# Optimization experiments

Hardware: AMD Instinct MI355X
Metric: run time of the kernel (lower is better)

The kernel has to match this reference:

```python
import jax, jax.numpy as jnp
import numpy as np

N = 500_000   # active voxels
K = 27        # 3x3x3 kernel offsets
CIN = 32
COUT = 64
EPS = 1e-5


def setup_inputs() -> dict:
    key = jax.random.key(0)
    ks = jax.random.split(key, 9)
    x_feats = jax.random.normal(ks[0], (N, CIN), jnp.float32)
    # neighbor map: for each kernel offset k and output voxel i, index of the
    # input voxel contributing through offset k (submanifold conv, stride=1)
    nbr = jax.random.randint(ks[1], (K, N), 0, N, jnp.int32)
    s1 = 1.0 / np.sqrt(K * CIN)
    s2 = 1.0 / np.sqrt(K * COUT)
    w1 = jax.random.normal(ks[2], (K, CIN, COUT), jnp.float32) * s1
    w2 = jax.random.normal(ks[3], (K, COUT, COUT), jnp.float32) * s2
    g1 = jnp.ones((COUT,), jnp.float32)
    b1 = jnp.zeros((COUT,), jnp.float32)
    g2 = jnp.ones((COUT,), jnp.float32)
    b2 = jnp.zeros((COUT,), jnp.float32)
    wid = jax.random.normal(ks[4], (CIN, COUT), jnp.float32) * (1.0 / np.sqrt(CIN))
    gid = jnp.ones((COUT,), jnp.float32)
    bid = jnp.zeros((COUT,), jnp.float32)
    return {"x_feats": x_feats, "nbr": nbr, "w1": w1, "g1": g1, "b1": b1,
            "w2": w2, "g2": g2, "b2": b2, "wid": wid, "gid": gid, "bid": bid}


def _sparse_conv(feats, nbr, W):
    # feats [N, Cin], nbr [K, N], W [K, Cin, Cout]
    # scan over the fixed 27 kernel offsets: gather -> matmul -> accumulate
    def step(acc, kw):
        idx, w = kw
        return acc + feats[idx] @ w, None
    out0 = jnp.zeros((feats.shape[0], W.shape[-1]), feats.dtype)
    out, _ = jax.lax.scan(step, out0, (nbr, W))
    return out


def _bn(x, g, b):
    # training-mode BatchNorm1d over the voxel axis (biased variance, as torch)
    m = jnp.mean(x, axis=0)
    v = jnp.var(x, axis=0)
    return (x - m) * jax.lax.rsqrt(v + EPS) * g + b


def reference(x_feats, nbr, w1, g1, b1, w2, g2, b2, wid, gid, bid):
    h = jax.nn.relu(_bn(_sparse_conv(x_feats, nbr, w1), g1, b1))
    h = _bn(_sparse_conv(h, nbr, w2), g2, b2)
    ident = _bn(x_feats @ wid, gid, bid)
    return jax.nn.relu(h + ident)
```

## Files before the change

kernel.cpp:

```cpp
#include <hip/hip_runtime.h>

#define NV 500000
#define KOFF 27
#define CIN_ 32
#define COUT_ 64
#define EPS_ 1e-5f

typedef __attribute__((ext_vector_type(8))) _Float16 half8;
typedef __attribute__((ext_vector_type(4))) float floatx4;


__global__ void zero_stats_kernel(float* __restrict__ s) {
  if (threadIdx.x < 384) s[threadIdx.x] = 0.f;
}

__global__ __launch_bounds__(256) void cast_x_kernel(
    const float* __restrict__ x, _Float16* __restrict__ xh) {
  size_t q = (size_t)blockIdx.x * 256 + threadIdx.x;
  if (q >= (size_t)NV * CIN_ / 8) return;
  const float4* xp = (const float4*)x;
  float4 a = xp[2 * q], b = xp[2 * q + 1];
  half8 h;
  h[0] = (_Float16)a.x; h[1] = (_Float16)a.y; h[2] = (_Float16)a.z; h[3] = (_Float16)a.w;
  h[4] = (_Float16)b.x; h[5] = (_Float16)b.y; h[6] = (_Float16)b.z; h[7] = (_Float16)b.w;
  ((half8*)xh)[q] = h;
}

__global__ void wtrans_kernel(const float* __restrict__ w,
                              _Float16* __restrict__ wT, int CI) {
  int t = blockIdx.x * 256 + threadIdx.x;
  int total = KOFF * CI * COUT_;
  if (t >= total) return;
  int k = t / (CI * COUT_);
  int r = t % (CI * COUT_);
  int co = r / CI;
  int ci = r % CI;
  wT[t] = (_Float16)w[(k * CI + ci) * COUT_ + co];
}


template<int CI>
__device__ __forceinline__ void stageB(const _Float16* __restrict__ wT,
                                       _Float16* __restrict__ lds,
                                       int k0, int kp, int tid) {
  __syncthreads();
  const int segs = CI / 8;
  const int chunks = kp * COUT_ * segs;
  for (int idx = tid; idx < chunks; idx += 1024) {
    int row = idx / segs;
    int s = idx - row * segs;
    half8 v = *(const half8*)(wT + ((size_t)k0 * COUT_ + row) * CI + s * 8);
    *(half8*)(lds + (size_t)row * (CI + 8) + s * 8) = v;
  }
  __syncthreads();
}

template<int CI, int KPC, int D>
__device__ __forceinline__ void run_phase(
    const half8* __restrict__ fp, const int* __restrict__ nbr,
    const _Float16* __restrict__ lds, int k0,
    int v0, int v1, int m, int quad, floatx4 acc[2][4]) {
  constexpr int SEG = CI / 32;
  constexpr int ROWH8 = CI / 8;

  int j0[KPC], j1[KPC];
#pragma unroll
  for (int k = 0; k < KPC; ++k) {
    j0[k] = nbr[(k0 + k) * NV + v0] * ROWH8;
    j1[k] = nbr[(k0 + k) * NV + v1] * ROWH8;
  }

  half8 ring[D][2][SEG];
#pragma unroll
  for (int p = 0; p < D; ++p) {
#pragma unroll
    for (int s = 0; s < SEG; ++s) {
      ring[p][0][s] = fp[(size_t)j0[p] + s * 4 + quad];
      ring[p][1][s] = fp[(size_t)j1[p] + s * 4 + quad];
    }
  }

#pragma unroll
  for (int k = 0; k < KPC; ++k) {
    const _Float16* bk = lds + (size_t)k * COUT_ * (CI + 8);
#pragma unroll
    for (int s = 0; s < SEG; ++s) {
#pragma unroll
      for (int nf = 0; nf < 4; ++nf) {
        half8 bf = *(const half8*)(bk + (nf * 16 + m) * (CI + 8) + s * 32 + quad * 8);
        acc[0][nf] = __builtin_amdgcn_mfma_f32_16x16x32_f16(ring[k % D][0][s], bf, acc[0][nf], 0, 0, 0);
        acc[1][nf] = __builtin_amdgcn_mfma_f32_16x16x32_f16(ring[k % D][1][s], bf, acc[1][nf], 0, 0, 0);
      }
    }
    if (k + D < KPC) {
#pragma unroll
      for (int s = 0; s < SEG; ++s) {
        ring[k % D][0][s] = fp[(size_t)j0[k + D] + s * 4 + quad];
        ring[k % D][1][s] = fp[(size_t)j1[k + D] + s * 4 + quad];
      }
    }
  }
}

template<int CI, bool WF16>
__global__ __launch_bounds__(1024, 4) void conv_mfma_v3(
    const _Float16* __restrict__ feats, const int* __restrict__ nbr,
    const _Float16* __restrict__ wT, float* __restrict__ outF,
    _Float16* __restrict__ outH) {
  constexpr int LDSH = (CI == 64) ? 7 * 64 * 72 : 9 * 64 * 40;
  __shared__ __align__(16) _Float16 ldsB[LDSH];

  int tid = threadIdx.x;
  int wave = tid >> 6, lane = tid & 63;
  int m = lane & 15, quad = lane >> 4;
  int vbase = (blockIdx.x * 16 + wave) * 32;
  int v0 = vbase + m;
  int v1 = vbase + 16 + m;
  v0 = v0 < NV ? v0 : NV - 1;
  v1 = v1 < NV ? v1 : NV - 1;
  const half8* fp = (const half8*)feats;

  floatx4 acc[2][4];
#pragma unroll
  for (int g = 0; g < 2; ++g)
#pragma unroll
    for (int nf = 0; nf < 4; ++nf) acc[g][nf] = (floatx4){0.f, 0.f, 0.f, 0.f};

  if constexpr (CI == 64) {
    stageB<CI>(wT, ldsB, 0, 7, tid);
    run_phase<CI, 7, 3>(fp, nbr, ldsB, 0, v0, v1, m, quad, acc);
    stageB<CI>(wT, ldsB, 7, 7, tid);
    run_phase<CI, 7, 3>(fp, nbr, ldsB, 7, v0, v1, m, quad, acc);
    stageB<CI>(wT, ldsB, 14, 7, tid);
    run_phase<CI, 7, 3>(fp, nbr, ldsB, 14, v0, v1, m, quad, acc);
    stageB<CI>(wT, ldsB, 21, 6, tid);
    run_phase<CI, 6, 3>(fp, nbr, ldsB, 21, v0, v1, m, quad, acc);
  } else {
    stageB<CI>(wT, ldsB, 0, 9, tid);
    run_phase<CI, 9, 4>(fp, nbr, ldsB, 0, v0, v1, m, quad, acc);
    stageB<CI>(wT, ldsB, 9, 9, tid);
    run_phase<CI, 9, 4>(fp, nbr, ldsB, 9, v0, v1, m, quad, acc);
    stageB<CI>(wT, ldsB, 18, 9, tid);
    run_phase<CI, 9, 4>(fp, nbr, ldsB, 18, v0, v1, m, quad, acc);
  }

#pragma unroll
  for (int g = 0; g < 2; ++g)
#pragma unroll
    for (int nf = 0; nf < 4; ++nf)
#pragma unroll
      for (int r = 0; r < 4; ++r) {
        int row = vbase + g * 16 + quad * 4 + r;
        if (row < NV) {
          size_t o = (size_t)row * COUT_ + nf * 16 + m;
          if (WF16) outH[o] = (_Float16)acc[g][nf][r];
          else outF[o] = acc[g][nf][r];
        }
      }
}


__global__ __launch_bounds__(256) void stats_f16_kernel(
    const _Float16* __restrict__ y, float* __restrict__ sums) {
  int lane = threadIdx.x & 63;
  int r0 = blockIdx.x * 4 + (threadIdx.x >> 6);
  int stride = gridDim.x * 4;
  float s = 0.f, ss = 0.f;
  for (int r = r0; r < NV; r += stride) {
    float v = (float)y[(size_t)r * COUT_ + lane];
    s += v;
    ss = fmaf(v, v, ss);
  }
  __shared__ float ls[128];
  if (threadIdx.x < 128) ls[threadIdx.x] = 0.f;
  __syncthreads();
  atomicAdd(&ls[lane], s);
  atomicAdd(&ls[64 + lane], ss);
  __syncthreads();
  if (threadIdx.x < 128) atomicAdd(&sums[threadIdx.x], ls[threadIdx.x]);
}

__global__ __launch_bounds__(256) void stats_f32_kernel(
    const float* __restrict__ y, float* __restrict__ sums) {
  int lane = threadIdx.x & 63;
  int r0 = blockIdx.x * 4 + (threadIdx.x >> 6);
  int stride = gridDim.x * 4;
  float s = 0.f, ss = 0.f;
  for (int r = r0; r < NV; r += stride) {
    float v = y[(size_t)r * COUT_ + lane];
    s += v;
    ss = fmaf(v, v, ss);
  }
  __shared__ float ls[128];
  if (threadIdx.x < 128) ls[threadIdx.x] = 0.f;
  __syncthreads();
  atomicAdd(&ls[lane], s);
  atomicAdd(&ls[64 + lane], ss);
  __syncthreads();
  if (threadIdx.x < 128) atomicAdd(&sums[threadIdx.x], ls[threadIdx.x]);
}

__global__ __launch_bounds__(256) void ident_stats_kernel(
    const float* __restrict__ x, const float* __restrict__ wid,
    float* __restrict__ sums) {
  int lane = threadIdx.x & 63;
  int wv = blockIdx.x * 4 + (threadIdx.x >> 6);
  int nw = gridDim.x * 4;
  float wcol[CIN_];
#pragma unroll
  for (int ci = 0; ci < CIN_; ++ci) wcol[ci] = wid[ci * COUT_ + lane];
  float s = 0.f, ss = 0.f;
  for (int v = wv; v < NV; v += nw) {
    const float* xr = x + (size_t)v * CIN_;
    float d = 0.f;
#pragma unroll
    for (int ci = 0; ci < CIN_; ++ci) d = fmaf(xr[ci], wcol[ci], d);
    s += d;
    ss = fmaf(d, d, ss);
  }
  __shared__ float ls[128];
  if (threadIdx.x < 128) ls[threadIdx.x] = 0.f;
  __syncthreads();
  atomicAdd(&ls[lane], s);
  atomicAdd(&ls[64 + lane], ss);
  __syncthreads();
  if (threadIdx.x < 128) atomicAdd(&sums[threadIdx.x], ls[threadIdx.x]);
}

__global__ void finalize_kernel(const float* __restrict__ sums,
                                const float* __restrict__ g,
                                const float* __restrict__ b,
                                float* __restrict__ out) {
  int c = threadIdx.x;
  float m = sums[c] * (1.0f / NV);
  float var = sums[64 + c] * (1.0f / NV) - m * m;
  float sc = g[c] / sqrtf(var + EPS_);
  out[c] = sc;
  out[64 + c] = b[c] - m * sc;
}

__global__ __launch_bounds__(256) void bnrelu_f16_kernel(
    _Float16* __restrict__ y, const float* __restrict__ scsh) {
  size_t q = (size_t)blockIdx.x * 256 + threadIdx.x;
  if (q >= (size_t)NV * COUT_ / 8) return;
  int c0 = (int)(q & 7) * 8;
  half8 v = ((const half8*)y)[q];
#pragma unroll
  for (int jj = 0; jj < 8; ++jj) {
    float f = fmaxf(fmaf((float)v[jj], scsh[c0 + jj], scsh[64 + c0 + jj]), 0.f);
    v[jj] = (_Float16)f;
  }
  ((half8*)y)[q] = v;
}

__global__ __launch_bounds__(256) void final_kernel(
    const float* __restrict__ x, const float* __restrict__ wid,
    float* __restrict__ y2out, const float* __restrict__ ss2,
    const float* __restrict__ ssid) {
  int lane = threadIdx.x & 63;
  int wv = blockIdx.x * 4 + (threadIdx.x >> 6);
  int nw = gridDim.x * 4;
  float wcol[CIN_];
#pragma unroll
  for (int ci = 0; ci < CIN_; ++ci) wcol[ci] = wid[ci * COUT_ + lane];
  float sc2 = ss2[lane], sh2 = ss2[64 + lane];
  float sci = ssid[lane], shi = ssid[64 + lane];
  for (int v = wv; v < NV; v += nw) {
    const float* xr = x + (size_t)v * CIN_;
    float d = 0.f;
#pragma unroll
    for (int ci = 0; ci < CIN_; ++ci) d = fmaf(xr[ci], wcol[ci], d);
    size_t o = (size_t)v * COUT_ + lane;
    float r = fmaf(y2out[o], sc2, sh2) + fmaf(d, sci, shi);
    y2out[o] = fmaxf(r, 0.f);
  }
}

extern "C" void kernel_launch(void* const* d_in, const int* in_sizes, int n_in,
                              void* d_out, int out_size, void* d_ws, size_t ws_size,
                              hipStream_t stream) {
  const float* x   = (const float*)d_in[0];
  const int*   nbr = (const int*)d_in[1];
  const float* w1  = (const float*)d_in[2];
  const float* g1  = (const float*)d_in[3];
  const float* b1  = (const float*)d_in[4];
  const float* w2  = (const float*)d_in[5];
  const float* g2  = (const float*)d_in[6];
  const float* b2  = (const float*)d_in[7];
  const float* wid = (const float*)d_in[8];
  const float* gid = (const float*)d_in[9];
  const float* bid = (const float*)d_in[10];
  float* out = (float*)d_out;

  _Float16* y1h = (_Float16*)d_ws;
  _Float16* xh  = y1h + (size_t)NV * COUT_;
  _Float16* wT1 = xh + (size_t)NV * CIN_;
  _Float16* wT2 = wT1 + KOFF * COUT_ * CIN_;
  float*    st  = (float*)(wT2 + KOFF * COUT_ * COUT_);

  const int NWG = (NV + 511) / 512;

  zero_stats_kernel<<<1, 384, 0, stream>>>(st);
  cast_x_kernel<<<(NV * CIN_ / 8 + 255) / 256, 256, 0, stream>>>(x, xh);
  wtrans_kernel<<<(KOFF * CIN_ * COUT_ + 255) / 256, 256, 0, stream>>>(w1, wT1, CIN_);
  wtrans_kernel<<<(KOFF * COUT_ * COUT_ + 255) / 256, 256, 0, stream>>>(w2, wT2, COUT_);

  conv_mfma_v3<CIN_, true><<<NWG, 1024, 0, stream>>>(xh, nbr, wT1, nullptr, y1h);
  stats_f16_kernel<<<2048, 256, 0, stream>>>(y1h, st + 0);
  ident_stats_kernel<<<2048, 256, 0, stream>>>(x, wid, st + 256);
  finalize_kernel<<<1, 64, 0, stream>>>(st + 0, g1, b1, st + 384);
  finalize_kernel<<<1, 64, 0, stream>>>(st + 256, gid, bid, st + 640);
  bnrelu_f16_kernel<<<(NV * COUT_ / 8 + 255) / 256, 256, 0, stream>>>(y1h, st + 384);

  conv_mfma_v3<COUT_, false><<<NWG, 1024, 0, stream>>>(y1h, nbr, wT2, out, nullptr);
  stats_f32_kernel<<<2048, 256, 0, stream>>>(out, st + 128);
  finalize_kernel<<<1, 64, 0, stream>>>(st + 128, g2, b2, st + 512);
  final_kernel<<<4096, 256, 0, stream>>>(x, wid, out, st + 512, st + 640);
}
```

Before: 1.182 ms.

## Fuse BN statistics into conv epilogues and pre-swizzle weights into MFMA fragment order

The BatchNorm sum and sum-of-squares reductions now happen in the conv kernel epilogues, using wave shuffles and LDS atomics, so the separate passes that re-read y1 and the output are gone. The x cast to fp16 is merged into the identity-branch stats kernel, and weight transposition plus stats zeroing go into a single prep kernel. That prep kernel writes weights in per-lane MFMA fragment order, so LDS staging becomes a plain contiguous copy and B-fragment reads are conflict-free. This removes several full-tensor memory passes and kernel launches, at the cost of extra epilogue work and atomics inside the conv kernels.

```diff
diff --git a/kernel.cpp b/kernel.cpp
--- a/kernel.cpp
+++ b/kernel.cpp
@@ -10,58 +10,94 @@
 typedef __attribute__((ext_vector_type(4))) float floatx4;
 
 
-__global__ void zero_stats_kernel(float* __restrict__ s) {
-  if (threadIdx.x < 384) s[threadIdx.x] = 0.f;
-}
-
-__global__ __launch_bounds__(256) void cast_x_kernel(
-    const float* __restrict__ x, _Float16* __restrict__ xh) {
-  size_t q = (size_t)blockIdx.x * 256 + threadIdx.x;
-  if (q >= (size_t)NV * CIN_ / 8) return;
-  const float4* xp = (const float4*)x;
-  float4 a = xp[2 * q], b = xp[2 * q + 1];
+template<int CI>
+__device__ __forceinline__ void fill_chunk(const float* __restrict__ w,
+                                           half8* __restrict__ wS, int t) {
+  constexpr int SEG = CI / 32;
+  int k = t / (SEG * 256);
+  int r = t - k * SEG * 256;
+  int s = r >> 8;
+  int nf = (r >> 6) & 3;
+  int lane = r & 63;
+  int m = lane & 15, quad = lane >> 4;
+  int co = nf * 16 + m;
+  int ci0 = s * 32 + quad * 8;
   half8 h;
-  h[0] = (_Float16)a.x; h[1] = (_Float16)a.y; h[2] = (_Float16)a.z; h[3] = (_Float16)a.w;
-  h[4] = (_Float16)b.x; h[5] = (_Float16)b.y; h[6] = (_Float16)b.z; h[7] = (_Float16)b.w;
-  ((half8*)xh)[q] = h;
-}
-
-__global__ void wtrans_kernel(const float* __restrict__ w,
-                              _Float16* __restrict__ wT, int CI) {
+#pragma unroll
+  for (int j = 0; j < 8; ++j)
+    h[j] = (_Float16)w[(size_t)(k * CI + ci0 + j) * COUT_ + co];
+  wS[t] = h;
+}
+
+__global__ __launch_bounds__(256) void prep_weights(
+    const float* __restrict__ w1, const float* __restrict__ w2,
+    _Float16* __restrict__ wS1, _Float16* __restrict__ wS2,
+    float* __restrict__ st) {
   int t = blockIdx.x * 256 + threadIdx.x;
-  int total = KOFF * CI * COUT_;
-  if (t >= total) return;
-  int k = t / (CI * COUT_);
-  int r = t % (CI * COUT_);
-  int co = r / CI;
-  int ci = r % CI;
-  wT[t] = (_Float16)w[(k * CI + ci) * COUT_ + co];
-}
-
-
-template<int CI>
-__device__ __forceinline__ void stageB(const _Float16* __restrict__ wT,
-                                       _Float16* __restrict__ lds,
+  if (t < 768) st[t] = 0.f;
+  const int T1 = KOFF * 256;
+  const int T2 = KOFF * 2 * 256;
+  if (t < T1) fill_chunk<32>(w1, (half8*)wS1, t);
+  else if (t < T1 + T2) fill_chunk<64>(w2, (half8*)wS2, t - T1);
+}
+
+__global__ __launch_bounds__(256) void prep_x(
+    const float* __restrict__ x, _Float16* __restrict__ xh,
+    const float* __restrict__ wid, float* __restrict__ st) {
+  int tid = threadIdx.x, lane = tid & 63;
+  int wv = blockIdx.x * 4 + (tid >> 6);
+  int nw = gridDim.x * 4;
+  float wcol[CIN_];
+#pragma unroll
+  for (int ci = 0; ci < CIN_; ++ci) wcol[ci] = wid[ci * COUT_ + lane];
+  half8* xh8 = (half8*)xh;
+  float s = 0.f, ss = 0.f;
+  for (int v = wv; v < NV; v += nw) {
+    const float* xr = x + (size_t)v * CIN_;
+    float xv[CIN_];
+#pragma unroll
+    for (int ci = 0; ci < CIN_; ++ci) xv[ci] = xr[ci];
+    float d = 0.f;
+#pragma unroll
+    for (int ci = 0; ci < CIN_; ++ci) d = fmaf(xv[ci], wcol[ci], d);
+    if (lane < 4) {
+      half8 h;
+#pragma unroll
+      for (int j = 0; j < 8; ++j) h[j] = (_Float16)xv[lane * 8 + j];
+      xh8[(size_t)v * 4 + lane] = h;
+    }
+    s += d;
+    ss = fmaf(d, d, ss);
+  }
+  __shared__ float ls[128];
+  if (tid < 128) ls[tid] = 0.f;
+  __syncthreads();
+  atomicAdd(&ls[lane], s);
+  atomicAdd(&ls[64 + lane], ss);
+  __syncthreads();
+  if (tid < 128) atomicAdd(&st[256 + tid], ls[tid]);
+}
+
+
+template<int SEG>
+__device__ __forceinline__ void stageW(const half8* __restrict__ wS,
+                                       half8* __restrict__ lds,
                                        int k0, int kp, int tid) {
   __syncthreads();
-  const int segs = CI / 8;
-  const int chunks = kp * COUT_ * segs;
-  for (int idx = tid; idx < chunks; idx += 1024) {
-    int row = idx / segs;
-    int s = idx - row * segs;
-    half8 v = *(const half8*)(wT + ((size_t)k0 * COUT_ + row) * CI + s * 8);
-    *(half8*)(lds + (size_t)row * (CI + 8) + s * 8) = v;
-  }
+  int chunks = kp * SEG * 256;
+  const half8* src = wS + k0 * SEG * 256;
+  for (int i = tid; i < chunks; i += 1024) lds[i] = src[i];
   __syncthreads();
 }
 
 template<int CI, int KPC, int D>
 __device__ __forceinline__ void run_phase(
     const half8* __restrict__ fp, const int* __restrict__ nbr,
-    const _Float16* __restrict__ lds, int k0,
-    int v0, int v1, int m, int quad, floatx4 acc[2][4]) {
+    const half8* __restrict__ lds, int k0,
+    int v0, int v1, int lane, floatx4 acc[2][4]) {
   constexpr int SEG = CI / 32;
   constexpr int ROWH8 = CI / 8;
+  int quad = lane >> 4;
 
   int j0[KPC], j1[KPC];
 #pragma unroll
@@ -72,22 +108,20 @@
 
   half8 ring[D][2][SEG];
 #pragma unroll
-  for (int p = 0; p < D; ++p) {
+  for (int p = 0; p < D; ++p)
 #pragma unroll
     for (int s = 0; s < SEG; ++s) {
       ring[p][0][s] = fp[(size_t)j0[p] + s * 4 + quad];
       ring[p][1][s] = fp[(size_t)j1[p] + s * 4 + quad];
     }
-  }
 
 #pragma unroll
   for (int k = 0; k < KPC; ++k) {
-    const _Float16* bk = lds + (size_t)k * COUT_ * (CI + 8);
 #pragma unroll
     for (int s = 0; s < SEG; ++s) {
 #pragma unroll
       for (int nf = 0; nf < 4; ++nf) {
-        half8 bf = *(const half8*)(bk + (nf * 16 + m) * (CI + 8) + s * 32 + quad * 8);
+        half8 bf = lds[((k * SEG + s) * 4 + nf) * 64 + lane];
         acc[0][nf] = __builtin_amdgcn_mfma_f32_16x16x32_f16(ring[k % D][0][s], bf, acc[0][nf], 0, 0, 0);
         acc[1][nf] = __builtin_amdgcn_mfma_f32_16x16x32_f16(ring[k % D][1][s], bf, acc[1][nf], 0, 0, 0);
       }
@@ -103,12 +137,13 @@
 }
 
 template<int CI, bool WF16>
-__global__ __launch_bounds__(1024, 4) void conv_mfma_v3(
+__global__ __launch_bounds__(1024, 4) void conv_mfma_v4(
     const _Float16* __restrict__ feats, const int* __restrict__ nbr,
-    const _Float16* __restrict__ wT, float* __restrict__ outF,
-    _Float16* __restrict__ outH) {
-  constexpr int LDSH = (CI == 64) ? 7 * 64 * 72 : 9 * 64 * 40;
-  __shared__ __align__(16) _Float16 ldsB[LDSH];
+    const _Float16* __restrict__ wS, float* __restrict__ outF,
+    _Float16* __restrict__ outH, float* __restrict__ stats) {
+  constexpr int SEG = CI / 32;
+  constexpr int LDSH8 = (CI == 64) ? 7 * 2 * 256 : 9 * 256;
+  __shared__ half8 ldsB[LDSH8];
 
   int tid = threadIdx.x;
   int wave = tid >> 6, lane = tid & 63;
@@ -119,6 +154,7 @@
   v0 = v0 < NV ? v0 : NV - 1;
   v1 = v1 < NV ? v1 : NV - 1;
   const half8* fp = (const half8*)feats;
+  const half8* wp = (const half8*)wS;
 
   floatx4 acc[2][4];
 #pragma unroll
@@ -127,104 +163,71 @@
     for (int nf = 0; nf < 4; ++nf) acc[g][nf] = (floatx4){0.f, 0.f, 0.f, 0.f};
 
   if constexpr (CI == 64) {
-    stageB<CI>(wT, ldsB, 0, 7, tid);
-    run_phase<CI, 7, 3>(fp, nbr, ldsB, 0, v0, v1, m, quad, acc);
-    stageB<CI>(wT, ldsB, 7, 7, tid);
-    run_phase<CI, 7, 3>(fp, nbr, ldsB, 7, v0, v1, m, quad, acc);
-    stageB<CI>(wT, ldsB, 14, 7, tid);
-    run_phase<CI, 7, 3>(fp, nbr, ldsB, 14, v0, v1, m, quad, acc);
-    stageB<CI>(wT, ldsB, 21, 6, tid);
-    run_phase<CI, 6, 3>(fp, nbr, ldsB, 21, v0, v1, m, quad, acc);
+    stageW<SEG>(wp, ldsB, 0, 7, tid);
+    run_phase<CI, 7, 3>(fp, nbr, ldsB, 0, v0, v1, lane, acc);
+    stageW<SEG>(wp, ldsB, 7, 7, tid);
+    run_phase<CI, 7, 3>(fp, nbr, ldsB, 7, v0, v1, lane, acc);
+    stageW<SEG>(wp, ldsB, 14, 7, tid);
+    run_phase<CI, 7, 3>(fp, nbr, ldsB, 14, v0, v1, lane, acc);
+    stageW<SEG>(wp, ldsB, 21, 6, tid);
+    run_phase<CI, 6, 3>(fp, nbr, ldsB, 21, v0, v1, lane, acc);
   } else {
-    stageB<CI>(wT, ldsB, 0, 9, tid);
-    run_phase<CI, 9, 4>(fp, nbr, ldsB, 0, v0, v1, m, quad, acc);
-    stageB<CI>(wT, ldsB, 9, 9, tid);
-    run_phase<CI, 9, 4>(fp, nbr, ldsB, 9, v0, v1, m, quad, acc);
-    stageB<CI>(wT, ldsB, 18, 9, tid);
-    run_phase<CI, 9, 4>(fp, nbr, ldsB, 18, v0, v1, m, quad, acc);
-  }
-
-#pragma unroll
-  for (int g = 0; g < 2; ++g)
-#pragma unroll
-    for (int nf = 0; nf < 4; ++nf)
+    stageW<SEG>(wp, ldsB, 0, 9, tid);
+    run_phase<CI, 9, 4>(fp, nbr, ldsB, 0, v0, v1, lane, acc);
+    stageW<SEG>(wp, ldsB, 9, 9, tid);
+    run_phase<CI, 9, 4>(fp, nbr, ldsB, 9, v0, v1, lane, acc);
+    stageW<SEG>(wp, ldsB, 18, 9, tid);
+    run_phase<CI, 9, 4>(fp, nbr, ldsB, 18, v0, v1, lane, acc);
+  }
+
+  __syncthreads();
+  float* ls = (float*)ldsB;
+  if (tid < 128) ls[tid] = 0.f;
+  __syncthreads();
+#pragma unroll
+  for (int nf = 0; nf < 4; ++nf) {
+    float s = 0.f, ss = 0.f;
+#pragma unroll
+    for (int g = 0; g < 2; ++g)
 #pragma unroll
       for (int r = 0; r < 4; ++r) {
         int row = vbase + g * 16 + quad * 4 + r;
         if (row < NV) {
+          float v = acc[g][nf][r];
           size_t o = (size_t)row * COUT_ + nf * 16 + m;
-          if (WF16) outH[o] = (_Float16)acc[g][nf][r];
-          else outF[o] = acc[g][nf][r];
+          if (WF16) outH[o] = (_Float16)v;
+          else outF[o] = v;
+          s += v;
+          ss = fmaf(v, v, ss);
         }
       }
-}
-
-
-__global__ __launch_bounds__(256) void stats_f16_kernel(
-    const _Float16* __restrict__ y, float* __restrict__ sums) {
-  int lane = threadIdx.x & 63;
-  int r0 = blockIdx.x * 4 + (threadIdx.x >> 6);
-  int stride = gridDim.x * 4;
-  float s = 0.f, ss = 0.f;
-  for (int r = r0; r < NV; r += stride) {
-    float v = (float)y[(size_t)r * COUT_ + lane];
-    s += v;
-    ss = fmaf(v, v, ss);
-  }
-  __shared__ float ls[128];
-  if (threadIdx.x < 128) ls[threadIdx.x] = 0.f;
-  __syncthreads();
-  atomicAdd(&ls[lane], s);
-  atomicAdd(&ls[64 + lane], ss);
-  __syncthreads();
-  if (threadIdx.x < 128) atomicAdd(&sums[threadIdx.x], ls[threadIdx.x]);
-}
-
-__global__ __launch_bounds__(256) void stats_f32_kernel(
-    const float* __restrict__ y, float* __restrict__ sums) {
-  int lane = threadIdx.x & 63;
-  int r0 = blockIdx.x * 4 + (threadIdx.x >> 6);
-  int stride = gridDim.x * 4;
-  float s = 0.f, ss = 0.f;
-  for (int r = r0; r < NV; r += stride) {
-    float v = y[(size_t)r * COUT_ + lane];
-    s += v;
-    ss = fmaf(v, v, ss);
-  }
-  __shared__ float ls[128];
-  if (threadIdx.x < 128) ls[threadIdx.x] = 0.f;
-  __syncthreads();
-  atomicAdd(&ls[lane], s);
-  atomicAdd(&ls[64 + lane], ss);
-  __syncthreads();
-  if (threadIdx.x < 128) atomicAdd(&sums[threadIdx.x], ls[threadIdx.x]);
-}
-
-__global__ __launch_bounds__(256) void ident_stats_kernel(
-    const float* __restrict__ x, const float* __restrict__ wid,
-    float* __restrict__ sums) {
-  int lane = threadIdx.x & 63;
-  int wv = blockIdx.x * 4 + (threadIdx.x >> 6);
-  int nw = gridDim.x * 4;
-  float wcol[CIN_];
-#pragma unroll
-  for (int ci = 0; ci < CIN_; ++ci) wcol[ci] = wid[ci * COUT_ + lane];
-  float s = 0.f, ss = 0.f;
-  for (int v = wv; v < NV; v += nw) {
-    const float* xr = x + (size_t)v * CIN_;
-    float d = 0.f;
-#pragma unroll
-    for (int ci = 0; ci < CIN_; ++ci) d = fmaf(xr[ci], wcol[ci], d);
-    s += d;
-    ss = fmaf(d, d, ss);
-  }
-  __shared__ float ls[128];
-  if (threadIdx.x < 128) ls[threadIdx.x] = 0.f;
-  __syncthreads();
-  atomicAdd(&ls[lane], s);
-  atomicAdd(&ls[64 + lane], ss);
-  __syncthreads();
-  if (threadIdx.x < 128) atomicAdd(&sums[threadIdx.x], ls[threadIdx.x]);
+    s += __shfl_xor(s, 16, 64);
+    s += __shfl_xor(s, 32, 64);
+    ss += __shfl_xor(ss, 16, 64);
+    ss += __shfl_xor(ss, 32, 64);
+    if (quad == 0) {
+      atomicAdd(&ls[nf * 16 + m], s);
+      atomicAdd(&ls[64 + nf * 16 + m], ss);
+    }
+  }
+  __syncthreads();
+  if (tid < 128) atomicAdd(&stats[tid], ls[tid]);
+}
+
+__global__ void finalize12(float* __restrict__ st,
+                           const float* __restrict__ g1, const float* __restrict__ b1,
+                           const float* __restrict__ gid, const float* __restrict__ bid) {
+  int t = threadIdx.x;
+  int c = t & 63;
+  const float* sums = (t < 64) ? st : st + 256;
+  const float* g = (t < 64) ? g1 : gid;
+  const float* b = (t < 64) ? b1 : bid;
+  float* o = (t < 64) ? st + 384 : st + 640;
+  float m = sums[c] * (1.0f / NV);
+  float var = sums[64 + c] * (1.0f / NV) - m * m;
+  float sc = g[c] / sqrtf(var + EPS_);
+  o[c] = sc;
+  o[64 + c] = b[c] - m * sc;
 }
 
 __global__ void finalize_kernel(const float* __restrict__ sums,
@@ -294,26 +297,18 @@
 
   _Float16* y1h = (_Float16*)d_ws;
   _Float16* xh  = y1h + (size_t)NV * COUT_;
-  _Float16* wT1 = xh + (size_t)NV * CIN_;
-  _Float16* wT2 = wT1 + KOFF * COUT_ * CIN_;
-  float*    st  = (float*)(wT2 + KOFF * COUT_ * COUT_);
+  _Float16* wS1 = xh + (size_t)NV * CIN_;
+  _Float16* wS2 = wS1 + (size_t)KOFF * 256 * 8;
+  float*    st  = (float*)(wS2 + (size_t)KOFF * 2 * 256 * 8);
 
   const int NWG = (NV + 511) / 512;
 
-  zero_stats_kernel<<<1, 384, 0, stream>>>(st);
-  cast_x_kernel<<<(NV * CIN_ / 8 + 255) / 256, 256, 0, stream>>>(x, xh);
-  wtrans_kernel<<<(KOFF * CIN_ * COUT_ + 255) / 256, 256, 0, stream>>>(w1, wT1, CIN_);
-  wtrans_kernel<<<(KOFF * COUT_ * COUT_ + 255) / 256, 256, 0, stream>>>(w2, wT2, COUT_);
-
-  conv_mfma_v3<CIN_, true><<<NWG, 1024, 0, stream>>>(xh, nbr, wT1, nullptr, y1h);
-  stats_f16_kernel<<<2048, 256, 0, stream>>>(y1h, st + 0);
-  ident_stats_kernel<<<2048, 256, 0, stream>>>(x, wid, st + 256);
-  finalize_kernel<<<1, 64, 0, stream>>>(st + 0, g1, b1, st + 384);
-  finalize_kernel<<<1, 64, 0, stream>>>(st + 256, gid, bid, st + 640);
+  prep_weights<<<81, 256, 0, stream>>>(w1, w2, wS1, wS2, st);
+  prep_x<<<512, 256, 0, stream>>>(x, xh, wid, st);
+  conv_mfma_v4<CIN_, true><<<NWG, 1024, 0, stream>>>(xh, nbr, wS1, nullptr, y1h, st + 0);
+  finalize12<<<1, 128, 0, stream>>>(st, g1, b1, gid, bid);
   bnrelu_f16_kernel<<<(NV * COUT_ / 8 + 255) / 256, 256, 0, stream>>>(y1h, st + 384);
-
-  conv_mfma_v3<COUT_, false><<<NWG, 1024, 0, stream>>>(y1h, nbr, wT2, out, nullptr);
-  stats_f32_kernel<<<2048, 256, 0, stream>>>(out, st + 128);
+  conv_mfma_v4<COUT_, false><<<NWG, 1024, 0, stream>>>(y1h, nbr, wS2, out, nullptr, st + 128);
   finalize_kernel<<<1, 64, 0, stream>>>(st + 128, g2, b2, st + 512);
   final_kernel<<<4096, 256, 0, stream>>>(x, wid, out, st + 512, st + 640);
 }
```

After: 1.490 ms. 26.1% more time.
